# Kernel optimization log

Measured on AMD Instinct MI355X. Metric: run time of the kernel, lower is better.

The kernel has to match this reference:

```python
import jax, jax.numpy as jnp
import numpy as np

N_AGT, N_CTX, E, D, NC = 100000, 10000, 1000000, 128, 2


def _gn(x, w, b, eps=1e-5):
    # GroupNorm(num_groups=1) on (N, C): normalize over channels, affine.
    m = jnp.mean(x, axis=-1, keepdims=True)
    v = jnp.mean((x - m) ** 2, axis=-1, keepdims=True)
    return (x - m) * jax.lax.rsqrt(v + eps) * w + b


def setup_inputs() -> dict:
    key = jax.random.key(0)
    ks = jax.random.split(key, 16)
    s = 0.05  # weight scale
    return {
        "agts": jax.random.normal(ks[0], (N_AGT, D), jnp.float32),
        "ctx": jax.random.normal(ks[1], (N_CTX, D), jnp.float32),
        "agt_ctrs": jax.random.normal(ks[2], (N_AGT, NC), jnp.float32),
        "ctx_ctrs": jax.random.normal(ks[3], (N_CTX, NC), jnp.float32),
        "hi": jax.random.randint(ks[4], (E,), 0, N_AGT, jnp.int32),
        "wi": jax.random.randint(ks[5], (E,), 0, N_CTX, jnp.int32),
        "dist_w1": jax.random.normal(ks[6], (D, NC), jnp.float32) * s,
        "dist_b1": jnp.zeros((D,), jnp.float32),
        "dist_w2": jax.random.normal(ks[7], (D, D), jnp.float32) * s,
        "dist_gw": jnp.ones((D,), jnp.float32),
        "dist_gb": jnp.zeros((D,), jnp.float32),
        "q_w": jax.random.normal(ks[8], (D, D), jnp.float32) * s,
        "q_gw": jnp.ones((D,), jnp.float32),
        "q_gb": jnp.zeros((D,), jnp.float32),
        "ctx_w1": jax.random.normal(ks[9], (D, 3 * D), jnp.float32) * s,
        "ctx_gw": jnp.ones((D,), jnp.float32),
        "ctx_gb": jnp.zeros((D,), jnp.float32),
        "ctx_w2": jax.random.normal(ks[10], (D, D), jnp.float32) * s,
        "agt_w": jax.random.normal(ks[11], (D, D), jnp.float32) * s,
        "norm_gw": jnp.ones((D,), jnp.float32),
        "norm_gb": jnp.zeros((D,), jnp.float32),
        "lin_w": jax.random.normal(ks[12], (D, D), jnp.float32) * s,
        "lin_gw": jnp.ones((D,), jnp.float32),
        "lin_gb": jnp.zeros((D,), jnp.float32),
    }


def reference(agts, ctx, agt_ctrs, ctx_ctrs, hi, wi,
              dist_w1, dist_b1, dist_w2, dist_gw, dist_gb,
              q_w, q_gw, q_gb,
              ctx_w1, ctx_gw, ctx_gb, ctx_w2,
              agt_w, norm_gw, norm_gb,
              lin_w, lin_gw, lin_gb):
    res = agts
    # per-edge relative displacement: [E, 2]
    d = agt_ctrs[hi] - ctx_ctrs[wi]
    # dist MLP: Linear(2,128)+ReLU, Linear(128,128,nobias)+GN+ReLU
    d = jax.nn.relu(d @ dist_w1.T + dist_b1)
    d = jax.nn.relu(_gn(d @ dist_w2.T, dist_gw, dist_gb))
    # query: Linear(128,128,nobias)+GN+ReLU on gathered agents
    q = jax.nn.relu(_gn(agts[hi] @ q_w.T, q_gw, q_gb))
    # concat-MLP over edges: [E, 384] -> [E, 128]
    c = jnp.concatenate([d, q, ctx[wi]], axis=1)
    c = jax.nn.relu(_gn(c @ ctx_w1.T, ctx_gw, ctx_gb))
    c = c @ ctx_w2.T
    # agent transform + index_add scatter of edge messages
    a = agts @ agt_w.T
    a = a.at[hi].add(c)
    a = jax.nn.relu(_gn(a, norm_gw, norm_gb))
    a = _gn(a @ lin_w.T, lin_gw, lin_gb)  # Linear block with act=False
    a = jax.nn.relu(a + res)
    return a
```

## Files before the change

### kernel.cpp

```cpp
#include <hip/hip_runtime.h>
#include <stdint.h>


#define N_AGT 100000
#define N_CTX 10000
#define NE    1000000
#define D     128

typedef __attribute__((ext_vector_type(8))) __bf16 bf16x8;
typedef __attribute__((ext_vector_type(4))) float f32x4;
typedef __attribute__((ext_vector_type(4))) unsigned int uint32x4;
typedef __attribute__((ext_vector_type(8))) unsigned short ushort8;

__device__ __forceinline__ float bf_lo(uint32_t u){ return __uint_as_float(u << 16); }
__device__ __forceinline__ float bf_hi(uint32_t u){ return __uint_as_float(u & 0xFFFF0000u); }
__device__ __forceinline__ uint16_t f2bf(float f){
  uint32_t u = __float_as_uint(f);
  u += 0x7FFFu + ((u >> 16) & 1u);
  return (uint16_t)(u >> 16);
}
__device__ __forceinline__ float bf2f(uint16_t v){ return __uint_as_float(((uint32_t)v) << 16); }

__device__ __forceinline__ f32x4 mfma16(bf16x8 a, bf16x8 b, f32x4 c){
  return __builtin_amdgcn_mfma_f32_16x16x32_bf16(a, b, c, 0, 0, 0);
}


__device__ __forceinline__ void stage_wsz(char* dst, const float* __restrict__ W,
                                          int rs, int co, int tid, int nthr){
  for (int idx = tid; idx < 128*16; idx += nthr){
    const int row = idx >> 4, ch = idx & 15;
    const float4 f0 = *(const float4*)(W + (size_t)row*rs + co + ch*8);
    const float4 f1 = *(const float4*)(W + (size_t)row*rs + co + ch*8 + 4);
    ushort8 u;
    u[0]=f2bf(f0.x); u[1]=f2bf(f0.y); u[2]=f2bf(f0.z); u[3]=f2bf(f0.w);
    u[4]=f2bf(f1.x); u[5]=f2bf(f1.y); u[6]=f2bf(f1.z); u[7]=f2bf(f1.w);
    *(uint32x4*)(dst + row*256 + ((ch*16) ^ ((row&7)<<4))) = __builtin_bit_cast(uint32x4, u);
  }
}

__device__ __forceinline__ bf16x8 ldfrag(const char* base, int row, int cb){
  return __builtin_bit_cast(bf16x8,
      *(const uint32x4*)(base + row*256 + (cb ^ ((row&7)<<4))));
}

__device__ __forceinline__ void mm_stage(const char* xb, const char* wm, int wv,
                                         int llo, int lhi, f32x4 acc[3][2]){
  #pragma unroll
  for (int kt = 0; kt < 4; kt++){
    const int cb = kt*64 + lhi*16;
    const bf16x8 b0 = ldfrag(wm, wv*32 + llo,      cb);
    const bf16x8 b1 = ldfrag(wm, wv*32 + 16 + llo, cb);
    #pragma unroll
    for (int mt = 0; mt < 3; mt++){
      const bf16x8 a = ldfrag(xb, mt*16 + llo, cb);
      acc[mt][0] = mfma16(a, b0, acc[mt][0]);
      acc[mt][1] = mfma16(a, b1, acc[mt][1]);
    }
  }
}

__device__ __forceinline__ void scat_acc(char* xb, const f32x4 acc[3][2],
                                         int wv, int llo, int lhi){
  #pragma unroll
  for (int mt = 0; mt < 3; mt++)
    #pragma unroll
    for (int ntl = 0; ntl < 2; ntl++)
      #pragma unroll
      for (int r = 0; r < 4; r++){
        const int m = mt*16 + lhi*4 + r;
        const int n = wv*32 + ntl*16 + llo;
        *(uint16_t*)(xb + m*256 + ((n*2) ^ ((m&7)<<4))) = f2bf(acc[mt][ntl][r]);
      }
}

__device__ __forceinline__ void gn_rowpass(char* xb, const int rr[3], int llo,
                                           const float gw[8], const float gb[8]){
  #pragma unroll
  for (int i = 0; i < 3; i++){
    const int row = rr[i];
    char* p = xb + row*256 + ((llo*16) ^ ((row&7)<<4));
    ushort8 u = __builtin_bit_cast(ushort8, *(const uint32x4*)p);
    float f[8]; float s = 0.f, ss = 0.f;
    #pragma unroll
    for (int j = 0; j < 8; j++){ f[j] = bf2f(u[j]); s += f[j]; ss += f[j]*f[j]; }
    #pragma unroll
    for (int m = 1; m < 16; m <<= 1){ s += __shfl_xor(s, m); ss += __shfl_xor(ss, m); }
    const float mean = s*(1.f/128.f);
    const float var  = ss*(1.f/128.f) - mean*mean;
    const float rstd = rsqrtf(var + 1e-5f);
    #pragma unroll
    for (int j = 0; j < 8; j++){
      const float g = fmaxf((f[j]-mean)*rstd*gw[j] + gb[j], 0.f);
      u[j] = f2bf(g);
    }
    *(uint32x4*)p = __builtin_bit_cast(uint32x4, u);
  }
}

__device__ __forceinline__ void gn_rowpass_add(char* xb, const int rr[3], int llo,
                                               const float gw[8], const float gb[8],
                                               const ushort8 qs[3]){
  #pragma unroll
  for (int i = 0; i < 3; i++){
    const int row = rr[i];
    char* p = xb + row*256 + ((llo*16) ^ ((row&7)<<4));
    ushort8 u = __builtin_bit_cast(ushort8, *(const uint32x4*)p);
    float f[8]; float s = 0.f, ss = 0.f;
    #pragma unroll
    for (int j = 0; j < 8; j++){
      f[j] = bf2f(u[j]) + bf2f(qs[i][j]);
      s += f[j]; ss += f[j]*f[j];
    }
    #pragma unroll
    for (int m = 1; m < 16; m <<= 1){ s += __shfl_xor(s, m); ss += __shfl_xor(ss, m); }
    const float mean = s*(1.f/128.f);
    const float var  = ss*(1.f/128.f) - mean*mean;
    const float rstd = rsqrtf(var + 1e-5f);
    #pragma unroll
    for (int j = 0; j < 8; j++){
      const float g = fmaxf((f[j]-mean)*rstd*gw[j] + gb[j], 0.f);
      u[j] = f2bf(g);
    }
    *(uint32x4*)p = __builtin_bit_cast(uint32x4, u);
  }
}

#define GE      96
#define NITER_E ((NE + GE - 1) / GE)

__global__ __launch_bounds__(512, 2) void k_edge_mfma(
    const float* __restrict__ agt_ctrs, const float* __restrict__ ctx_ctrs,
    const int* __restrict__ hi, const int* __restrict__ wi,
    const float* __restrict__ dist_w1, const float* __restrict__ dist_b1,
    const float* __restrict__ dist_gw, const float* __restrict__ dist_gb,
    const float* __restrict__ ctx_gw, const float* __restrict__ ctx_gb,
    const float* __restrict__ dist_w2, const float* __restrict__ ctx_w1,
    const float* __restrict__ ctx_w2,
    const uint16_t* __restrict__ QW, const uint16_t* __restrict__ CtxP,
    float* __restrict__ A0){
  extern __shared__ __align__(16) char smem[];
  const int tid  = threadIdx.x;
  const int wave = tid >> 6, lane = tid & 63;
  const int grp  = wave >> 2, wv = wave & 3;
  const int lhi  = lane >> 4, llo = lane & 15;

  stage_wsz(smem,         dist_w2, 128, 0, tid, 512);
  stage_wsz(smem + 32768, ctx_w1,  384, 0, tid, 512);
  stage_wsz(smem + 65536, ctx_w2,  128, 0, tid, 512);

  char* xb = smem + 98304 + grp*12288;
  int*  hb = (int*)(smem + 122880) + grp*96;

  const int c0 = llo*8;
  float w1x[8], w1y[8], b1v[8], dgw[8], dgb[8], cgw[8], cgb[8];
  #pragma unroll
  for (int j = 0; j < 8; j++){
    w1x[j] = dist_w1[(c0+j)*2 + 0];
    w1y[j] = dist_w1[(c0+j)*2 + 1];
    b1v[j] = dist_b1[c0+j];
    dgw[j] = dist_gw[c0+j]; dgb[j] = dist_gb[c0+j];
    cgw[j] = ctx_gw[c0+j];  cgb[j] = ctx_gb[c0+j];
  }

  int rr[3];
  #pragma unroll
  for (int i = 0; i < 3; i++) rr[i] = wv*12 + i*4 + lhi;

  ushort8 qg[3], cg[3];
  float2 acs[3], ccs[3];

  const long step = gridDim.x;
  long it = blockIdx.x;
  if (it < NITER_E){
    const long ebase = it*GE + grp*48;
    #pragma unroll
    for (int i = 0; i < 3; i++){
      long e = ebase + rr[i]; if (e >= NE) e = NE - 1;
      const int h = hi[e], w = wi[e];
      qg[i]  = *(const ushort8*)&QW  [(size_t)h*D + c0];
      cg[i]  = *(const ushort8*)&CtxP[(size_t)w*D + c0];
      acs[i] = *(const float2*)&agt_ctrs[(size_t)h*2];
      ccs[i] = *(const float2*)&ctx_ctrs[(size_t)w*2];
    }
    if (wv == 0 && lane < 48){
      long e = ebase + lane; if (e >= NE) e = NE - 1;
      hb[lane] = hi[e];
    }
  }
  __syncthreads();

  int pb = 0;
  for (; it < NITER_E; it += step, pb ^= 1){
    const long ebase = it*GE + grp*48;
    ushort8 qs[3];
    #pragma unroll
    for (int i = 0; i < 3; i++){
      const float dx = acs[i].x - ccs[i].x, dy = acs[i].y - ccs[i].y;
      ushort8 u;
      #pragma unroll
      for (int j = 0; j < 8; j++)
        u[j] = f2bf(fmaxf(fmaf(dx, w1x[j], fmaf(dy, w1y[j], b1v[j])), 0.f));
      *(uint32x4*)(xb + rr[i]*256 + ((llo*16) ^ ((rr[i]&7)<<4))) =
          __builtin_bit_cast(uint32x4, u);
      ushort8 v;
      #pragma unroll
      for (int j = 0; j < 8; j++) v[j] = f2bf(bf2f(qg[i][j]) + bf2f(cg[i][j]));
      qs[i] = v;
    }
    const long nit = it + step;
    if (nit < NITER_E){
      const long nbase = nit*GE + grp*48;
      #pragma unroll
      for (int i = 0; i < 3; i++){
        long e = nbase + rr[i]; if (e >= NE) e = NE - 1;
        const int h = hi[e], w = wi[e];
        qg[i]  = *(const ushort8*)&QW  [(size_t)h*D + c0];
        cg[i]  = *(const ushort8*)&CtxP[(size_t)w*D + c0];
        acs[i] = *(const float2*)&agt_ctrs[(size_t)h*2];
        ccs[i] = *(const float2*)&ctx_ctrs[(size_t)w*2];
      }
      if (wv == 0 && lane < 48){
        long e = nbase + lane; if (e >= NE) e = NE - 1;
        hb[(pb^1)*48 + lane] = hi[e];
      }
    }
    __syncthreads();
    f32x4 acc1[3][2];
    #pragma unroll
    for (int mt = 0; mt < 3; mt++){ acc1[mt][0] = (f32x4)0.f; acc1[mt][1] = (f32x4)0.f; }
    mm_stage(xb, smem, wv, llo, lhi, acc1);
    __syncthreads();
    scat_acc(xb, acc1, wv, llo, lhi);
    __syncthreads();
    gn_rowpass(xb, rr, llo, dgw, dgb);
    __syncthreads();
    f32x4 acc2[3][2];
    #pragma unroll
    for (int mt = 0; mt < 3; mt++){ acc2[mt][0] = (f32x4)0.f; acc2[mt][1] = (f32x4)0.f; }
    mm_stage(xb, smem + 32768, wv, llo, lhi, acc2);
    __syncthreads();
    scat_acc(xb, acc2, wv, llo, lhi);
    __syncthreads();
    gn_rowpass_add(xb, rr, llo, cgw, cgb, qs);
    __syncthreads();
    f32x4 acc3[3][2];
    #pragma unroll
    for (int mt = 0; mt < 3; mt++){ acc3[mt][0] = (f32x4)0.f; acc3[mt][1] = (f32x4)0.f; }
    mm_stage(xb, smem + 65536, wv, llo, lhi, acc3);
    #pragma unroll
    for (int mt = 0; mt < 3; mt++)
      #pragma unroll
      for (int ntl = 0; ntl < 2; ntl++)
        #pragma unroll
        for (int r = 0; r < 4; r++){
          const int m = mt*16 + lhi*4 + r;
          if (ebase + m < NE){
            const int n = wv*32 + ntl*16 + llo;
            atomicAdd(&A0[(size_t)hb[pb*48 + m]*D + n], acc3[mt][ntl][r]);
          }
        }
    __syncthreads();
  }
}

#define NITER_A ((N_AGT + 95) / 96)

__global__ __launch_bounds__(512, 2) void k_agent_pre_mfma(
    const float* __restrict__ agts, const float* __restrict__ q_w,
    const float* __restrict__ ctx_w1, const float* __restrict__ agt_w,
    const float* __restrict__ q_gw, const float* __restrict__ q_gb,
    uint16_t* __restrict__ QW, float* __restrict__ A0){
  extern __shared__ __align__(16) char smem[];
  const int tid  = threadIdx.x;
  const int wave = tid >> 6, lane = tid & 63;
  const int grp  = wave >> 2, wv = wave & 3;
  const int lhi  = lane >> 4, llo = lane & 15;

  stage_wsz(smem,         q_w,    128, 0,   tid, 512);
  stage_wsz(smem + 32768, agt_w,  128, 0,   tid, 512);
  stage_wsz(smem + 65536, ctx_w1, 384, 128, tid, 512);

  char* xb = smem + 98304 + grp*12288;
  const int c0 = llo*8;
  float qgw[8], qgb[8];
  #pragma unroll
  for (int j = 0; j < 8; j++){ qgw[j] = q_gw[c0+j]; qgb[j] = q_gb[c0+j]; }
  __syncthreads();

  const int tg = tid & 255;
  int rr[3];
  #pragma unroll
  for (int i = 0; i < 3; i++) rr[i] = wv*12 + i*4 + lhi;

  for (int it = blockIdx.x; it < NITER_A; it += gridDim.x){
    const int rbase = it*96 + grp*48;
    for (int idx = tg; idx < 48*32; idx += 256){
      const int row = idx >> 5, c4 = idx & 31;
      int gr = rbase + row; if (gr >= N_AGT) gr = N_AGT - 1;
      const float4 f = *(const float4*)(agts + (size_t)gr*D + c4*4);
      const uint32_t lo = ((uint32_t)f2bf(f.y) << 16) | (uint32_t)f2bf(f.x);
      const uint32_t hi2 = ((uint32_t)f2bf(f.w) << 16) | (uint32_t)f2bf(f.z);
      *(uint2*)(xb + row*256 + ((c4*8) ^ ((row&7)<<4))) = make_uint2(lo, hi2);
    }
    __syncthreads();
    f32x4 acc[3][2];
    #pragma unroll
    for (int mt = 0; mt < 3; mt++){ acc[mt][0] = (f32x4)0.f; acc[mt][1] = (f32x4)0.f; }
    mm_stage(xb, smem + 32768, wv, llo, lhi, acc);
    #pragma unroll
    for (int mt = 0; mt < 3; mt++)
      #pragma unroll
      for (int ntl = 0; ntl < 2; ntl++)
        #pragma unroll
        for (int r = 0; r < 4; r++){
          const int m = mt*16 + lhi*4 + r;
          if (rbase + m < N_AGT){
            const int n = wv*32 + ntl*16 + llo;
            A0[(size_t)(rbase + m)*D + n] = acc[mt][ntl][r];
          }
        }
    #pragma unroll
    for (int mt = 0; mt < 3; mt++){ acc[mt][0] = (f32x4)0.f; acc[mt][1] = (f32x4)0.f; }
    mm_stage(xb, smem, wv, llo, lhi, acc);
    __syncthreads();
    scat_acc(xb, acc, wv, llo, lhi);
    __syncthreads();
    gn_rowpass(xb, rr, llo, qgw, qgb);
    __syncthreads();
    #pragma unroll
    for (int mt = 0; mt < 3; mt++){ acc[mt][0] = (f32x4)0.f; acc[mt][1] = (f32x4)0.f; }
    mm_stage(xb, smem + 65536, wv, llo, lhi, acc);
    __syncthreads();
    scat_acc(xb, acc, wv, llo, lhi);
    __syncthreads();
    #pragma unroll
    for (int i = 0; i < 3; i++){
      const int row = rr[i], gr = rbase + row;
      if (gr < N_AGT){
        const uint32x4 u = *(const uint32x4*)(xb + row*256 + ((llo*16) ^ ((row&7)<<4)));
        *(uint32x4*)(QW + (size_t)gr*D + c0) = u;
      }
    }
    __syncthreads();
  }
}

__global__ __launch_bounds__(512, 4) void k_post_mfma(
    float* __restrict__ A0, const float* __restrict__ agts,
    const float* __restrict__ lin_w,
    const float* __restrict__ norm_gw, const float* __restrict__ norm_gb,
    const float* __restrict__ lin_gw, const float* __restrict__ lin_gb){
  extern __shared__ __align__(16) char smem[];
  const int tid  = threadIdx.x;
  const int wave = tid >> 6, lane = tid & 63;
  const int grp  = wave >> 2, wv = wave & 3;
  const int lhi  = lane >> 4, llo = lane & 15;

  stage_wsz(smem, lin_w, 128, 0, tid, 512);
  char* xb = smem + 32768 + grp*12288;
  const int c0 = llo*8;
  float ngw[8], ngb[8], lgw[8], lgb[8];
  #pragma unroll
  for (int j = 0; j < 8; j++){
    ngw[j] = norm_gw[c0+j]; ngb[j] = norm_gb[c0+j];
    lgw[j] = lin_gw[c0+j];  lgb[j] = lin_gb[c0+j];
  }
  __syncthreads();

  int rr[3];
  #pragma unroll
  for (int i = 0; i < 3; i++) rr[i] = wv*12 + i*4 + lhi;

  for (int it = blockIdx.x; it < NITER_A; it += gridDim.x){
    const int rbase = it*96 + grp*48;
    #pragma unroll
    for (int i = 0; i < 3; i++){
      const int row = rr[i];
      int gr = rbase + row; if (gr >= N_AGT) gr = N_AGT - 1;
      const float4 a0 = *(const float4*)(A0 + (size_t)gr*D + c0);
      const float4 a1 = *(const float4*)(A0 + (size_t)gr*D + c0 + 4);
      float f[8] = {a0.x,a0.y,a0.z,a0.w,a1.x,a1.y,a1.z,a1.w};
      float s = 0.f, ss = 0.f;
      #pragma unroll
      for (int j = 0; j < 8; j++){ s += f[j]; ss += f[j]*f[j]; }
      #pragma unroll
      for (int m = 1; m < 16; m <<= 1){ s += __shfl_xor(s, m); ss += __shfl_xor(ss, m); }
      const float mean = s*(1.f/128.f);
      const float var  = ss*(1.f/128.f) - mean*mean;
      const float rstd = rsqrtf(var + 1e-5f);
      ushort8 u;
      #pragma unroll
      for (int j = 0; j < 8; j++)
        u[j] = f2bf(fmaxf((f[j]-mean)*rstd*ngw[j] + ngb[j], 0.f));
      *(uint32x4*)(xb + row*256 + ((llo*16) ^ ((row&7)<<4))) =
          __builtin_bit_cast(uint32x4, u);
    }
    __syncthreads();
    f32x4 acc[3][2];
    #pragma unroll
    for (int mt = 0; mt < 3; mt++){ acc[mt][0] = (f32x4)0.f; acc[mt][1] = (f32x4)0.f; }
    mm_stage(xb, smem, wv, llo, lhi, acc);
    __syncthreads();
    scat_acc(xb, acc, wv, llo, lhi);
    __syncthreads();
    #pragma unroll
    for (int i = 0; i < 3; i++){
      const int row = rr[i];
      const char* p = xb + row*256 + ((llo*16) ^ ((row&7)<<4));
      const ushort8 u = __builtin_bit_cast(ushort8, *(const uint32x4*)p);
      float f[8]; float s = 0.f, ss = 0.f;
      #pragma unroll
      for (int j = 0; j < 8; j++){ f[j] = bf2f(u[j]); s += f[j]; ss += f[j]*f[j]; }
      #pragma unroll
      for (int m = 1; m < 16; m <<= 1){ s += __shfl_xor(s, m); ss += __shfl_xor(ss, m); }
      const float mean = s*(1.f/128.f);
      const float var  = ss*(1.f/128.f) - mean*mean;
      const float rstd = rsqrtf(var + 1e-5f);
      const int gr = rbase + row;
      if (gr < N_AGT){
        const float4 r0 = *(const float4*)(agts + (size_t)gr*D + c0);
        const float4 r1 = *(const float4*)(agts + (size_t)gr*D + c0 + 4);
        const float res[8] = {r0.x,r0.y,r0.z,r0.w,r1.x,r1.y,r1.z,r1.w};
        float o[8];
        float4 o0, o1;
        #pragma unroll
        for (int j = 0; j < 8; j++)
          o[j] = fmaxf((f[j]-mean)*rstd*lgw[j] + lgb[j] + res[j], 0.f);
        o0.x=o[0]; o0.y=o[1]; o0.z=o[2]; o0.w=o[3];
        o1.x=o[4]; o1.y=o[5]; o1.z=o[6]; o1.w=o[7];
        *(float4*)(A0 + (size_t)gr*D + c0)     = o0;
        *(float4*)(A0 + (size_t)gr*D + c0 + 4) = o1;
      }
    }
    __syncthreads();
  }
}

__device__ __forceinline__ void stage_w4(uint32_t* wp, const float* __restrict__ W,
                                         int rs, int co, int tid, int nthr){
  for (int idx = tid; idx < 32*128; idx += nthr){
    int p2 = idx & 31, o = idx >> 5;
    const float4 f = *(const float4*)(W + (size_t)o*rs + co + p2*4);
    uint32_t lo = ((uint32_t)f2bf(f.y) << 16) | (uint32_t)f2bf(f.x);
    uint32_t hi = ((uint32_t)f2bf(f.w) << 16) | (uint32_t)f2bf(f.z);
    *(uint2*)&wp[(p2*128 + o)*2] = make_uint2(lo, hi);
  }
}

__device__ __forceinline__ float dot128(const uint32_t* wp, const float* xb, int o){
  float acc = 0.f;
  #pragma unroll 8
  for (int p2 = 0; p2 < 32; p2++){
    const uint2 w = *(const uint2*)&wp[(p2*128 + o)*2];
    const float4 x = *(const float4*)&xb[p2*4];
    acc += x.x*bf_lo(w.x) + x.y*bf_hi(w.x) + x.z*bf_lo(w.y) + x.w*bf_hi(w.y);
  }
  return acc;
}

__global__ __launch_bounds__(128) void k_ctx(const float* __restrict__ ctx,
                                             const float* __restrict__ ctx_w1,
                                             uint16_t* __restrict__ CtxP){
  __shared__ __align__(16) uint32_t wc[32*128*2];
  __shared__ __align__(16) float xbuf[128];
  const int tid = threadIdx.x;
  stage_w4(wc, ctx_w1, 384, 256, tid, 128);
  __syncthreads();
  for (int row = blockIdx.x; row < N_CTX; row += gridDim.x){
    __syncthreads();
    xbuf[tid] = ctx[(size_t)row*D + tid];
    __syncthreads();
    const float acc = dot128(wc, xbuf, tid);
    CtxP[(size_t)row*D + tid] = f2bf(acc);
  }
}

extern "C" void kernel_launch(void* const* d_in, const int* in_sizes, int n_in,
                              void* d_out, int out_size, void* d_ws, size_t ws_size,
                              hipStream_t stream){
  const float* agts     = (const float*)d_in[0];
  const float* ctx      = (const float*)d_in[1];
  const float* agt_ctrs = (const float*)d_in[2];
  const float* ctx_ctrs = (const float*)d_in[3];
  const int*   hi       = (const int*)d_in[4];
  const int*   wi       = (const int*)d_in[5];
  const float* dist_w1  = (const float*)d_in[6];
  const float* dist_b1  = (const float*)d_in[7];
  const float* dist_w2  = (const float*)d_in[8];
  const float* dist_gw  = (const float*)d_in[9];
  const float* dist_gb  = (const float*)d_in[10];
  const float* q_w      = (const float*)d_in[11];
  const float* q_gw     = (const float*)d_in[12];
  const float* q_gb     = (const float*)d_in[13];
  const float* ctx_w1   = (const float*)d_in[14];
  const float* ctx_gw   = (const float*)d_in[15];
  const float* ctx_gb   = (const float*)d_in[16];
  const float* ctx_w2   = (const float*)d_in[17];
  const float* agt_w    = (const float*)d_in[18];
  const float* norm_gw  = (const float*)d_in[19];
  const float* norm_gb  = (const float*)d_in[20];
  const float* lin_w    = (const float*)d_in[21];
  const float* lin_gw   = (const float*)d_in[22];
  const float* lin_gb   = (const float*)d_in[23];

  uint16_t* QW   = (uint16_t*)d_ws;
  uint16_t* CtxP = QW + (size_t)N_AGT * D;
  float*    A0   = (float*)d_out;

  const int EDGE_LDS = 123648;
  const int APRE_LDS = 122880;
  const int POST_LDS = 57344;
  hipFuncSetAttribute((const void*)k_edge_mfma,
                      hipFuncAttributeMaxDynamicSharedMemorySize, EDGE_LDS);
  hipFuncSetAttribute((const void*)k_agent_pre_mfma,
                      hipFuncAttributeMaxDynamicSharedMemorySize, APRE_LDS);
  hipFuncSetAttribute((const void*)k_post_mfma,
                      hipFuncAttributeMaxDynamicSharedMemorySize, POST_LDS);

  k_ctx<<<1024, 128, 0, stream>>>(ctx, ctx_w1, CtxP);
  k_agent_pre_mfma<<<256, 512, APRE_LDS, stream>>>(agts, q_w, ctx_w1, agt_w,
      q_gw, q_gb, QW, A0);
  k_edge_mfma<<<256, 512, EDGE_LDS, stream>>>(agt_ctrs, ctx_ctrs, hi, wi,
      dist_w1, dist_b1, dist_gw, dist_gb, ctx_gw, ctx_gb,
      dist_w2, ctx_w1, ctx_w2, QW, CtxP, A0);
  k_post_mfma<<<512, 512, POST_LDS, stream>>>(A0, agts, lin_w,
      norm_gw, norm_gb, lin_gw, lin_gb);
}
```

Baseline: 658.6 us.

## Ping-pong edge-tile LDS buffers and use LDS-only barriers in edge kernel

The edge kernel's per-group activation tile is split into two LDS buffers (A/B). Each MFMA stage now reads one buffer while its accumulators are scattered into the other. This removes the barrier that separated each matmul from its scatter, cutting per-iteration barriers from seven to five. __syncthreads is also replaced by a custom barrier that waits only on LDS counters (lgkmcnt), so prefetched global gathers for the next iteration can stay in flight across barriers. The cost is about 24KB more dynamic LDS per block, plus reliance on hand-placed wait counts for correctness.

```diff
diff --git a/kernel.cpp b/kernel.cpp
--- a/kernel.cpp
+++ b/kernel.cpp
@@ -23,6 +23,12 @@
 
 __device__ __forceinline__ f32x4 mfma16(bf16x8 a, bf16x8 b, f32x4 c){
   return __builtin_amdgcn_mfma_f32_16x16x32_bf16(a, b, c, 0, 0, 0);
+}
+
+__device__ __forceinline__ void bar_lds(){
+  asm volatile("s_waitcnt lgkmcnt(0)" ::: "memory");
+  __builtin_amdgcn_s_barrier();
+  __builtin_amdgcn_sched_barrier(0);
 }
 
 
@@ -149,8 +155,9 @@
   stage_wsz(smem + 32768, ctx_w1,  384, 0, tid, 512);
   stage_wsz(smem + 65536, ctx_w2,  128, 0, tid, 512);
 
-  char* xb = smem + 98304 + grp*12288;
-  int*  hb = (int*)(smem + 122880) + grp*96;
+  char* xbA = smem + 98304 + grp*24576;
+  char* xbB = xbA + 12288;
+  int*  hb  = (int*)(smem + 147456) + grp*96;
 
   const int c0 = llo*8;
   float w1x[8], w1y[8], b1v[8], dgw[8], dgb[8], cgw[8], cgb[8];
@@ -201,7 +208,7 @@
       #pragma unroll
       for (int j = 0; j < 8; j++)
         u[j] = f2bf(fmaxf(fmaf(dx, w1x[j], fmaf(dy, w1y[j], b1v[j])), 0.f));
-      *(uint32x4*)(xb + rr[i]*256 + ((llo*16) ^ ((rr[i]&7)<<4))) =
+      *(uint32x4*)(xbA + rr[i]*256 + ((llo*16) ^ ((rr[i]&7)<<4))) =
           __builtin_bit_cast(uint32x4, u);
       ushort8 v;
       #pragma unroll
@@ -225,29 +232,27 @@
         hb[(pb^1)*48 + lane] = hi[e];
       }
     }
-    __syncthreads();
+    bar_lds();
     f32x4 acc1[3][2];
     #pragma unroll
     for (int mt = 0; mt < 3; mt++){ acc1[mt][0] = (f32x4)0.f; acc1[mt][1] = (f32x4)0.f; }
-    mm_stage(xb, smem, wv, llo, lhi, acc1);
-    __syncthreads();
-    scat_acc(xb, acc1, wv, llo, lhi);
-    __syncthreads();
-    gn_rowpass(xb, rr, llo, dgw, dgb);
-    __syncthreads();
+    mm_stage(xbA, smem, wv, llo, lhi, acc1);
+    scat_acc(xbB, acc1, wv, llo, lhi);
+    bar_lds();
+    gn_rowpass(xbB, rr, llo, dgw, dgb);
+    bar_lds();
     f32x4 acc2[3][2];
     #pragma unroll
     for (int mt = 0; mt < 3; mt++){ acc2[mt][0] = (f32x4)0.f; acc2[mt][1] = (f32x4)0.f; }
-    mm_stage(xb, smem + 32768, wv, llo, lhi, acc2);
-    __syncthreads();
-    scat_acc(xb, acc2, wv, llo, lhi);
-    __syncthreads();
-    gn_rowpass_add(xb, rr, llo, cgw, cgb, qs);
-    __syncthreads();
+    mm_stage(xbB, smem + 32768, wv, llo, lhi, acc2);
+    scat_acc(xbA, acc2, wv, llo, lhi);
+    bar_lds();
+    gn_rowpass_add(xbA, rr, llo, cgw, cgb, qs);
+    bar_lds();
     f32x4 acc3[3][2];
     #pragma unroll
     for (int mt = 0; mt < 3; mt++){ acc3[mt][0] = (f32x4)0.f; acc3[mt][1] = (f32x4)0.f; }
-    mm_stage(xb, smem + 65536, wv, llo, lhi, acc3);
+    mm_stage(xbA, smem + 65536, wv, llo, lhi, acc3);
     #pragma unroll
     for (int mt = 0; mt < 3; mt++)
       #pragma unroll
@@ -260,7 +265,7 @@
             atomicAdd(&A0[(size_t)hb[pb*48 + m]*D + n], acc3[mt][ntl][r]);
           }
         }
-    __syncthreads();
+    bar_lds();
   }
 }
 
@@ -508,7 +513,7 @@
   uint16_t* CtxP = QW + (size_t)N_AGT * D;
   float*    A0   = (float*)d_out;
 
-  const int EDGE_LDS = 123648;
+  const int EDGE_LDS = 148224;
   const int APRE_LDS = 122880;
   const int POST_LDS = 57344;
   hipFuncSetAttribute((const void*)k_edge_mfma,
```

Measured after the change: 676.5 us. +2.7%, slower.
